# Kernel optimization log

Measured on AMD Instinct MI355X. Metric: run time of the kernel, lower is better.

Reference implementation:

```python
import jax, jax.numpy as jnp
import numpy as np

DIST_THRESH = 2.0
YAW_THRESH = np.pi / 3
PI = np.pi


def setup_inputs() -> dict:
    key = jax.random.key(0)
    k1, k2, k3 = jax.random.split(key, 3)
    B, K, T = 32, 16, 30
    N, n = 128, 20
    preds = jax.random.normal(k1, (B, K, T, 2), dtype=jnp.float32)
    centerline_nodes = jax.random.normal(k2, (B, N, n, 2), dtype=jnp.float32)
    centerline_node_masks = jax.random.randint(k3, (B, N, n), 0, 2, dtype=jnp.int32)
    return {
        "preds": preds,
        "centerline_nodes": centerline_nodes,
        "centerline_node_masks": centerline_node_masks,
    }


def _yaw_from_traj(traj):
    # traj: (..., L, 2) -> yaw (..., L), first element zero
    dv = traj[..., 1:, :] - traj[..., :-1, :]
    yaw = -jnp.arctan2(dv[..., 0], dv[..., 1])
    zeros = jnp.zeros(yaw.shape[:-1] + (1,), dtype=yaw.dtype)
    return jnp.concatenate([zeros, yaw], axis=-1)


def reference(preds, centerline_nodes, centerline_node_masks):
    B, K, T, _ = preds.shape
    pred_yaw = _yaw_from_traj(preds)                  # (B, K, T)
    node_yaw = _yaw_from_traj(centerline_nodes)       # (B, N, n)

    cn = centerline_nodes.reshape(B, -1, 2)           # (B, Nn, 2)
    mask = centerline_node_masks.reshape(B, -1)       # (B, Nn)
    pts = preds.reshape(B, -1, 2)                     # (B, KT, 2)

    # pairwise euclidean distance via ||a||^2 + ||b||^2 - 2 a.b
    a2 = jnp.sum(cn * cn, axis=-1)                    # (B, Nn)
    b2 = jnp.sum(pts * pts, axis=-1)                  # (B, KT)
    d2 = a2[:, :, None] + b2[:, None, :] - 2.0 * jnp.einsum("bnd,bkd->bnk", cn, pts)
    dists = jnp.sqrt(jnp.maximum(d2, 0.0))            # (B, Nn, KT)
    dists = jnp.where((mask == 1)[:, :, None], jnp.inf, dists)

    yaw_diffs = node_yaw.reshape(B, -1)[:, :, None] - pred_yaw.reshape(B, -1)[:, None, :]
    yaw_diffs = (yaw_diffs + PI) % (2.0 * PI) - PI    # wrap to [-pi, pi)

    cost = jax.nn.relu(dists - DIST_THRESH) + jax.nn.relu(jnp.abs(yaw_diffs) - YAW_THRESH)
    consistency = jnp.min(cost, axis=1)               # (B, KT)
    return consistency.reshape(B, K, T).sum(axis=-1)  # (B, K)
```

## Files before the change

kernel.cpp:

```cpp
#include <hip/hip_runtime.h>
#include <math.h>

#define B_     32
#define K_     16
#define T_     30
#define KT_    480
#define N_     128
#define NPN_   20
#define NODES_ 2560
#define CH_    16
#define CSZ_   160

#define PI_F      3.14159265358979323846f
#define TWO_PI_F  6.28318530717958647692f
#define YAW_TH_F  (PI_F / 3.0f)

__global__ __launch_bounds__(256) void cm_partial(
    const float* __restrict__ preds,
    const float* __restrict__ cn,
    const int*   __restrict__ cmask,
    float*       __restrict__ ws)
{
  const int b   = blockIdx.x / CH_;
  const int c   = blockIdx.x % CH_;
  const int tid = threadIdx.x;

  __shared__ float4 nd[CSZ_];

  if (tid < CSZ_) {
    const int gn = c * CSZ_ + tid;
    const int j  = gn % NPN_;
    const float2* cnb = (const float2*)cn + (size_t)b * NODES_;
    const float2 p = cnb[gn];
    float yaw = 0.0f;
    if (j != 0) {
      const float2 q = cnb[gn - 1];
      yaw = -atan2f(p.x - q.x, p.y - q.y);
    }
    const int mv = cmask[(size_t)b * NODES_ + gn];
    const float a2 = (mv == 1) ? INFINITY : fmaf(p.x, p.x, p.y * p.y);
    nd[tid] = make_float4(p.x, p.y, a2, yaw);
  }

  const int kt0 = tid;
  const int kt1 = tid + 256;
  const float2* pb = (const float2*)preds + (size_t)b * KT_;

  float px20, py20, cb0, pyaw0;
  float px21, py21, cb1, pyaw1;
  {
    const float2 pp = pb[kt0];
    pyaw0 = 0.0f;
    if ((kt0 % T_) != 0) {
      const float2 pq = pb[kt0 - 1];
      pyaw0 = -atan2f(pp.x - pq.x, pp.y - pq.y);
    }
    cb0  = fmaf(pp.x, pp.x, pp.y * pp.y);
    px20 = -2.0f * pp.x;
    py20 = -2.0f * pp.y;
  }
  if (kt1 < KT_) {
    const float2 pp = pb[kt1];
    pyaw1 = 0.0f;
    if ((kt1 % T_) != 0) {
      const float2 pq = pb[kt1 - 1];
      pyaw1 = -atan2f(pp.x - pq.x, pp.y - pq.y);
    }
    cb1  = fmaf(pp.x, pp.x, pp.y * pp.y);
    px21 = -2.0f * pp.x;
    py21 = -2.0f * pp.y;
  } else {
    pyaw1 = 0.0f; cb1 = 0.0f; px21 = 0.0f; py21 = 0.0f;
  }

  __syncthreads();

  float m0 = INFINITY, m1 = INFINITY;
  #pragma unroll 4
  for (int i = 0; i < CSZ_; ++i) {
    const float4 nv = nd[i];
    {
      float d2 = fmaf(nv.y, py20, fmaf(nv.x, px20, nv.z + cb0));
      d2 = fmaxf(d2, 0.0f);
      const float dist = __builtin_amdgcn_sqrtf(d2);
      const float yd = fabsf(nv.w - pyaw0);
      const float a  = fminf(yd, TWO_PI_F - yd);
      const float cost = fmaxf(dist - 2.0f, 0.0f) + fmaxf(a - YAW_TH_F, 0.0f);
      m0 = fminf(m0, cost);
    }
    {
      float d2 = fmaf(nv.y, py21, fmaf(nv.x, px21, nv.z + cb1));
      d2 = fmaxf(d2, 0.0f);
      const float dist = __builtin_amdgcn_sqrtf(d2);
      const float yd = fabsf(nv.w - pyaw1);
      const float a  = fminf(yd, TWO_PI_F - yd);
      const float cost = fmaxf(dist - 2.0f, 0.0f) + fmaxf(a - YAW_TH_F, 0.0f);
      m1 = fminf(m1, cost);
    }
  }

  ws[((size_t)b * KT_ + kt0) * CH_ + c] = m0;
  if (kt1 < KT_) ws[((size_t)b * KT_ + kt1) * CH_ + c] = m1;
}

__global__ __launch_bounds__(512) void cm_reduce(
    const float* __restrict__ ws, float* __restrict__ out)
{
  const int b   = blockIdx.x;
  const int tid = threadIdx.x;
  __shared__ float sc[KT_];

  if (tid < KT_) {
    const float4* w4 = (const float4*)(ws + ((size_t)b * KT_ + tid) * CH_);
    const float4 v0 = w4[0], v1 = w4[1], v2 = w4[2], v3 = w4[3];
    const float m =
      fminf(fminf(fminf(fminf(v0.x, v0.y), fminf(v0.z, v0.w)),
                  fminf(fminf(v1.x, v1.y), fminf(v1.z, v1.w))),
            fminf(fminf(fminf(v2.x, v2.y), fminf(v2.z, v2.w)),
                  fminf(fminf(v3.x, v3.y), fminf(v3.z, v3.w))));
    sc[tid] = m;
  }
  __syncthreads();

  if (tid < K_) {
    float s = 0.0f;
    #pragma unroll
    for (int t = 0; t < T_; ++t) s += sc[tid * T_ + t];
    out[b * K_ + tid] = s;
  }
}

extern "C" void kernel_launch(void* const* d_in, const int* in_sizes, int n_in,
                              void* d_out, int out_size, void* d_ws, size_t ws_size,
                              hipStream_t stream) {
  const float* preds = (const float*)d_in[0];
  const float* cn    = (const float*)d_in[1];
  const int*   cmask = (const int*)d_in[2];
  float* out = (float*)d_out;
  float* ws  = (float*)d_ws;

  cm_partial<<<dim3(B_ * CH_), dim3(256), 0, stream>>>(preds, cn, cmask, ws);
  cm_reduce<<<dim3(B_), dim3(512), 0, stream>>>(ws, out);
}
```

Measured before the change: 77.42 us.

## Split node/point preprocessing into a prep kernel and simplify inner cost loop

Adds a prep kernel that computes node and point features (yaw via atan2, squared norms, masked inf) once into workspace, so the main kernel no longer recomputes point atan2 in every chunk block. The main kernel uses twice as many chunks of half the size and folds the distance threshold algebraically: it clamps d2 at 4 instead of 0 and subtracts 2 after the min in the reduce. Partial minima are stored chunk-major so the reduce reads them coalesced. The cost is an extra kernel launch and a workspace round trip.

After: 75.99 us. Within noise of the previous version (-1.8%).

```diff
diff --git a/kernel.cpp b/kernel.cpp
--- a/kernel.cpp
+++ b/kernel.cpp
@@ -8,117 +8,125 @@
 #define N_     128
 #define NPN_   20
 #define NODES_ 2560
-#define CH_    16
-#define CSZ_   160
+#define CH_    32
+#define CSZ_   80
 
 #define PI_F      3.14159265358979323846f
 #define TWO_PI_F  6.28318530717958647692f
 #define YAW_TH_F  (PI_F / 3.0f)
 
-__global__ __launch_bounds__(256) void cm_partial(
+#define NNODE_TOT (B_ * NODES_)
+#define NPT_TOT   (B_ * KT_)
+
+#define WS_PTS_OFF   NNODE_TOT
+#define WS_PART_OFF4 (NNODE_TOT + NPT_TOT)
+
+__global__ __launch_bounds__(256) void cm_prep(
     const float* __restrict__ preds,
     const float* __restrict__ cn,
     const int*   __restrict__ cmask,
-    float*       __restrict__ ws)
+    float4*      __restrict__ ws)
 {
-  const int b   = blockIdx.x / CH_;
-  const int c   = blockIdx.x % CH_;
+  const int idx = blockIdx.x * 256 + threadIdx.x;
+  if (idx < NNODE_TOT) {
+    const int b  = idx / NODES_;
+    const int g  = idx - b * NODES_;
+    const int j  = g % NPN_;
+    const float2* cnb = (const float2*)cn + (size_t)b * NODES_;
+    const float2 p = cnb[g];
+    float yaw = 0.0f;
+    if (j != 0) {
+      const float2 q = cnb[g - 1];
+      yaw = -atan2f(p.x - q.x, p.y - q.y);
+    }
+    const int mv = cmask[idx];
+    const float a2 = (mv == 1) ? INFINITY : fmaf(p.x, p.x, p.y * p.y);
+    ws[idx] = make_float4(-2.0f * p.x, -2.0f * p.y, a2, yaw);
+  } else {
+    const int i2 = idx - NNODE_TOT;
+    const int b  = i2 / KT_;
+    const int kt = i2 - b * KT_;
+    const float2* pb = (const float2*)preds + (size_t)b * KT_;
+    const float2 pp = pb[kt];
+    float pyaw = 0.0f;
+    if ((kt % T_) != 0) {
+      const float2 pq = pb[kt - 1];
+      pyaw = -atan2f(pp.x - pq.x, pp.y - pq.y);
+    }
+    const float b2 = fmaf(pp.x, pp.x, pp.y * pp.y);
+    ws[WS_PTS_OFF + i2] = make_float4(pp.x, pp.y, b2, pyaw);
+  }
+}
+
+__global__ __launch_bounds__(256) void cm_main(
+    const float4* __restrict__ ws_nodes,
+    const float4* __restrict__ ws_pts,
+    float*        __restrict__ ws_part)
+{
+  const int b   = blockIdx.x >> 5;
+  const int c   = blockIdx.x & (CH_ - 1);
   const int tid = threadIdx.x;
 
   __shared__ float4 nd[CSZ_];
-
   if (tid < CSZ_) {
-    const int gn = c * CSZ_ + tid;
-    const int j  = gn % NPN_;
-    const float2* cnb = (const float2*)cn + (size_t)b * NODES_;
-    const float2 p = cnb[gn];
-    float yaw = 0.0f;
-    if (j != 0) {
-      const float2 q = cnb[gn - 1];
-      yaw = -atan2f(p.x - q.x, p.y - q.y);
-    }
-    const int mv = cmask[(size_t)b * NODES_ + gn];
-    const float a2 = (mv == 1) ? INFINITY : fmaf(p.x, p.x, p.y * p.y);
-    nd[tid] = make_float4(p.x, p.y, a2, yaw);
+    nd[tid] = ws_nodes[(size_t)b * NODES_ + c * CSZ_ + tid];
   }
 
   const int kt0 = tid;
   const int kt1 = tid + 256;
-  const float2* pb = (const float2*)preds + (size_t)b * KT_;
-
-  float px20, py20, cb0, pyaw0;
-  float px21, py21, cb1, pyaw1;
-  {
-    const float2 pp = pb[kt0];
-    pyaw0 = 0.0f;
-    if ((kt0 % T_) != 0) {
-      const float2 pq = pb[kt0 - 1];
-      pyaw0 = -atan2f(pp.x - pq.x, pp.y - pq.y);
-    }
-    cb0  = fmaf(pp.x, pp.x, pp.y * pp.y);
-    px20 = -2.0f * pp.x;
-    py20 = -2.0f * pp.y;
-  }
-  if (kt1 < KT_) {
-    const float2 pp = pb[kt1];
-    pyaw1 = 0.0f;
-    if ((kt1 % T_) != 0) {
-      const float2 pq = pb[kt1 - 1];
-      pyaw1 = -atan2f(pp.x - pq.x, pp.y - pq.y);
-    }
-    cb1  = fmaf(pp.x, pp.x, pp.y * pp.y);
-    px21 = -2.0f * pp.x;
-    py21 = -2.0f * pp.y;
-  } else {
-    pyaw1 = 0.0f; cb1 = 0.0f; px21 = 0.0f; py21 = 0.0f;
-  }
-
+  const float4 p0 = ws_pts[(size_t)b * KT_ + kt0];
+  const float4 p1 = (kt1 < KT_) ? ws_pts[(size_t)b * KT_ + kt1]
+                                : make_float4(0.f, 0.f, 0.f, 0.f);
   __syncthreads();
 
   float m0 = INFINITY, m1 = INFINITY;
-  #pragma unroll 4
+  #pragma unroll 8
   for (int i = 0; i < CSZ_; ++i) {
     const float4 nv = nd[i];
     {
-      float d2 = fmaf(nv.y, py20, fmaf(nv.x, px20, nv.z + cb0));
-      d2 = fmaxf(d2, 0.0f);
-      const float dist = __builtin_amdgcn_sqrtf(d2);
-      const float yd = fabsf(nv.w - pyaw0);
-      const float a  = fminf(yd, TWO_PI_F - yd);
-      const float cost = fmaxf(dist - 2.0f, 0.0f) + fmaxf(a - YAW_TH_F, 0.0f);
-      m0 = fminf(m0, cost);
+      float t = nv.z + p0.z;
+      t = fmaf(nv.x, p0.x, t);
+      t = fmaf(nv.y, p0.y, t);
+      t = fmaxf(t, 4.0f);
+      const float s  = __builtin_amdgcn_sqrtf(t);
+      const float yd = nv.w - p0.w;
+      const float w2 = TWO_PI_F - fabsf(yd);
+      const float a  = fminf(fabsf(yd), w2);
+      const float yc = fmaxf(a - YAW_TH_F, 0.0f);
+      m0 = fminf(m0, s + yc);
     }
     {
-      float d2 = fmaf(nv.y, py21, fmaf(nv.x, px21, nv.z + cb1));
-      d2 = fmaxf(d2, 0.0f);
-      const float dist = __builtin_amdgcn_sqrtf(d2);
-      const float yd = fabsf(nv.w - pyaw1);
-      const float a  = fminf(yd, TWO_PI_F - yd);
-      const float cost = fmaxf(dist - 2.0f, 0.0f) + fmaxf(a - YAW_TH_F, 0.0f);
-      m1 = fminf(m1, cost);
+      float t = nv.z + p1.z;
+      t = fmaf(nv.x, p1.x, t);
+      t = fmaf(nv.y, p1.y, t);
+      t = fmaxf(t, 4.0f);
+      const float s  = __builtin_amdgcn_sqrtf(t);
+      const float yd = nv.w - p1.w;
+      const float w2 = TWO_PI_F - fabsf(yd);
+      const float a  = fminf(fabsf(yd), w2);
+      const float yc = fmaxf(a - YAW_TH_F, 0.0f);
+      m1 = fminf(m1, s + yc);
     }
   }
 
-  ws[((size_t)b * KT_ + kt0) * CH_ + c] = m0;
-  if (kt1 < KT_) ws[((size_t)b * KT_ + kt1) * CH_ + c] = m1;
+  float* wp = ws_part + ((size_t)b * CH_ + c) * KT_;
+  wp[kt0] = m0;
+  if (kt1 < KT_) wp[kt1] = m1;
 }
 
 __global__ __launch_bounds__(512) void cm_reduce(
-    const float* __restrict__ ws, float* __restrict__ out)
+    const float* __restrict__ ws_part, float* __restrict__ out)
 {
   const int b   = blockIdx.x;
   const int tid = threadIdx.x;
   __shared__ float sc[KT_];
 
   if (tid < KT_) {
-    const float4* w4 = (const float4*)(ws + ((size_t)b * KT_ + tid) * CH_);
-    const float4 v0 = w4[0], v1 = w4[1], v2 = w4[2], v3 = w4[3];
-    const float m =
-      fminf(fminf(fminf(fminf(v0.x, v0.y), fminf(v0.z, v0.w)),
-                  fminf(fminf(v1.x, v1.y), fminf(v1.z, v1.w))),
-            fminf(fminf(fminf(v2.x, v2.y), fminf(v2.z, v2.w)),
-                  fminf(fminf(v3.x, v3.y), fminf(v3.z, v3.w))));
-    sc[tid] = m;
+    const float* wp = ws_part + (size_t)b * CH_ * KT_;
+    float m = INFINITY;
+    #pragma unroll
+    for (int c = 0; c < CH_; ++c) m = fminf(m, wp[c * KT_ + tid]);
+    sc[tid] = m - 2.0f;
   }
   __syncthreads();
 
@@ -137,8 +145,12 @@
   const float* cn    = (const float*)d_in[1];
   const int*   cmask = (const int*)d_in[2];
   float* out = (float*)d_out;
-  float* ws  = (float*)d_ws;
+  float4* ws4 = (float4*)d_ws;
+  float*  ws_part = (float*)(ws4 + WS_PART_OFF4);
 
-  cm_partial<<<dim3(B_ * CH_), dim3(256), 0, stream>>>(preds, cn, cmask, ws);
-  cm_reduce<<<dim3(B_), dim3(512), 0, stream>>>(ws, out);
+  cm_prep<<<dim3((NNODE_TOT + NPT_TOT) / 256), dim3(256), 0, stream>>>(
+      preds, cn, cmask, ws4);
+  cm_main<<<dim3(B_ * CH_), dim3(256), 0, stream>>>(
+      ws4, ws4 + WS_PTS_OFF, ws_part);
+  cm_reduce<<<dim3(B_), dim3(512), 0, stream>>>(ws_part, out);
 }
```
